# Kernel optimization log

Measured on AMD Instinct MI355X. Metric: run time of the kernel, lower is better.

Reference implementation:

```python
import jax, jax.numpy as jnp
import numpy as np

N_NODES = 100000
N_EDGES = 1600000
N_GRAPHS = 256
IN_C = 64
HID = 128
OUT = 128
BN_EPS = 1e-5


def setup_inputs() -> dict:
    key = jax.random.key(0)
    ks = jax.random.split(key, 24)
    x = jax.random.normal(ks[0], (N_NODES, IN_C), jnp.float32)
    edge_index = jax.random.randint(ks[1], (2, N_EDGES), 0, N_NODES, dtype=jnp.int64 if jax.config.jax_enable_x64 else jnp.int32)
    batch = jnp.sort(jax.random.randint(ks[2], (N_NODES,), 0, N_GRAPHS))

    def lin(k, i, o):
        return (jax.random.normal(k, (i, o), jnp.float32) / np.float32(np.sqrt(i)))

    d = {"x": x, "edge_index": edge_index, "batch": batch}
    in_dims = [IN_C, HID, HID]
    for l in range(3):
        d[f"w1_{l}"] = lin(ks[3 + 6 * l], in_dims[l], HID)
        d[f"b1_{l}"] = jnp.zeros((HID,), jnp.float32)
        d[f"w2_{l}"] = lin(ks[4 + 6 * l], HID, HID)
        d[f"b2_{l}"] = jnp.zeros((HID,), jnp.float32)
        d[f"gamma_{l}"] = jnp.ones((HID,), jnp.float32)
        d[f"beta_{l}"] = jnp.zeros((HID,), jnp.float32)
    d["proj_w"] = lin(ks[22], HID, OUT)
    d["proj_b"] = jnp.zeros((OUT,), jnp.float32)
    return d


def _gin_forward(x, edge_index, batch, layers, proj_w, proj_b):
    src, dst = edge_index[0], edge_index[1]
    h = x
    for (w1, b1, w2, b2, g, b) in layers:
        # GINConv (eps=0, aggr='add'): MLP(h_i + sum_{j->i} h_j)
        agg = jax.ops.segment_sum(h[src], dst, num_segments=h.shape[0])
        z = h + agg
        z = jax.nn.relu(z @ w1 + b1) @ w2 + b2
        # BatchNorm1d, training mode (biased batch stats)
        mean = z.mean(axis=0)
        var = z.var(axis=0)
        z = (z - mean) * jax.lax.rsqrt(var + BN_EPS) * g + b
        h = jax.nn.relu(z)
    # global_mean_pool over graph ids
    s = jax.ops.segment_sum(h, batch, num_segments=N_GRAPHS)
    cnt = jax.ops.segment_sum(jnp.ones((h.shape[0], 1), h.dtype), batch, num_segments=N_GRAPHS)
    hg = s / jnp.maximum(cnt, 1.0)
    return hg @ proj_w + proj_b


def reference(x, edge_index, batch,
              w1_0, b1_0, w2_0, b2_0, gamma_0, beta_0,
              w1_1, b1_1, w2_1, b2_1, gamma_1, beta_1,
              w1_2, b1_2, w2_2, b2_2, gamma_2, beta_2,
              proj_w, proj_b):
    layers = [
        (w1_0, b1_0, w2_0, b2_0, gamma_0, beta_0),
        (w1_1, b1_1, w2_1, b2_1, gamma_1, beta_1),
        (w1_2, b1_2, w2_2, b2_2, gamma_2, beta_2),
    ]
    return _gin_forward(x, edge_index, batch, layers, proj_w, proj_b)
```

## Files before the change

kernel.cpp:

```cpp
#include <hip/hip_runtime.h>

#define N_NODES 100000
#define N_EDGES 1600000
#define N_GRAPHS 256
#define HID 128
#define BN_EPS 1e-5f

#define NT 1563
#define EB 4096
#define RB 391
#define MB 1563

typedef __bf16 bf16x8 __attribute__((ext_vector_type(8)));
typedef __bf16 bf16x4 __attribute__((ext_vector_type(4)));
typedef __bf16 bf16x2 __attribute__((ext_vector_type(2)));
typedef float f32x4 __attribute__((ext_vector_type(4)));

__global__ __launch_bounds__(256) void setup_kernel(
    const float* __restrict__ x, __bf16* __restrict__ xb,
    const float* __restrict__ wa, const float* __restrict__ wb,
    const float* __restrict__ wc, const float* __restrict__ wd,
    const float* __restrict__ we, const float* __restrict__ wf,
    __bf16* __restrict__ wt,
    const int* __restrict__ batch, int* __restrict__ counts) {
  int b = blockIdx.x;
  if (b < 6250) {
    int idx = b * 256 + threadIdx.x;
    if (idx >= N_NODES * 16) return;
    f32x4 v = ((const f32x4*)x)[idx];
    bf16x4 o = {(__bf16)v[0], (__bf16)v[1], (__bf16)v[2], (__bf16)v[3]};
    ((bf16x4*)xb)[idx] = o;
  } else if (b < 6250 + 352) {
    int idx = (b - 6250) * 256 + threadIdx.x;
    if (idx >= 90112) return;
    const float* w;
    int K, local;
    if (idx < 8192) { w = wa; K = 64; local = idx; }
    else {
      int s = (idx - 8192) / 16384;
      local = (idx - 8192) - s * 16384;
      K = 128;
      w = (s == 0) ? wb : (s == 1) ? wc : (s == 2) ? wd : (s == 3) ? we : wf;
    }
    int n = local / K, k = local - n * K;
    wt[idx] = (__bf16)w[k * 128 + n];
  } else {
    int t = (b - 6602) * 256 + threadIdx.x;
    int r0 = t * 64;
    if (r0 >= N_NODES) return;
    int rend = min(r0 + 64, N_NODES);
    int curg = batch[r0], cnt = 0;
    for (int r = r0; r < rend; r++) {
      int g = batch[r];
      if (g != curg) {
        atomicAdd(&counts[curg], cnt);
        curg = g;
        cnt = 1;
      } else {
        cnt++;
      }
    }
    atomicAdd(&counts[curg], cnt);
  }
}

__global__ __launch_bounds__(256) void tile_hist_kernel(const int* __restrict__ ei,
                                                        int* __restrict__ tcnt) {
  __shared__ int hist[NT];
  int t = threadIdx.x;
  for (int i = t; i < NT; i += 256) hist[i] = 0;
  __syncthreads();
  int base = blockIdx.x * EB;
#pragma unroll 4
  for (int i = 0; i < EB / 256; i++) {
    int e = base + i * 256 + t;
    if (e < N_EDGES) atomicAdd(&hist[ei[N_EDGES + e] >> 6], 1);
  }
  __syncthreads();
  for (int i = t; i < NT; i += 256) {
    int h = hist[i];
    if (h) atomicAdd(&tcnt[i], h);
  }
}

__global__ __launch_bounds__(256) void tile_scan_kernel(const int* __restrict__ tcnt,
                                                        int* __restrict__ tstart,
                                                        int* __restrict__ gcursor) {
  __shared__ int ps[256];
  int t = threadIdx.x;
  const int CH = (NT + 255) / 256;
  int lo = t * CH, hi = min(lo + CH, NT);
  int s = 0;
  for (int i = lo; i < hi; i++) s += tcnt[i];
  ps[t] = s;
  __syncthreads();
  for (int off = 1; off < 256; off <<= 1) {
    int v = ps[t];
    int u = (t >= off) ? ps[t - off] : 0;
    __syncthreads();
    ps[t] = v + u;
    __syncthreads();
  }
  int base = (t == 0) ? 0 : ps[t - 1];
  for (int i = lo; i < hi; i++) {
    tstart[i] = base;
    gcursor[i] = base;
    base += tcnt[i];
  }
  if (t == 0) tstart[NT] = N_EDGES;
}

__global__ __launch_bounds__(256) void reorder2_kernel(const int* __restrict__ ei,
                                                       int* __restrict__ gcursor,
                                                       int* __restrict__ epack) {
  __shared__ int hist[NT];
  int t = threadIdx.x;
  for (int i = t; i < NT; i += 256) hist[i] = 0;
  __syncthreads();
  int base = blockIdx.x * EB;
#pragma unroll 4
  for (int i = 0; i < EB / 256; i++) {
    int e = base + i * 256 + t;
    if (e < N_EDGES) atomicAdd(&hist[ei[N_EDGES + e] >> 6], 1);
  }
  __syncthreads();
  for (int i = t; i < NT; i += 256) {
    int h = hist[i];
    if (h) hist[i] = atomicAdd(&gcursor[i], h);
  }
  __syncthreads();
#pragma unroll 4
  for (int i = 0; i < EB / 256; i++) {
    int e = base + i * 256 + t;
    if (e < N_EDGES) {
      int d = ei[N_EDGES + e];
      int s = ei[e];
      int pos = atomicAdd(&hist[d >> 6], 1);
      epack[pos] = (s << 6) | (d & 63);
    }
  }
}

__global__ __launch_bounds__(256) void row_sort_kernel(const int* __restrict__ tstart,
                                                       const int* __restrict__ epack,
                                                       int* __restrict__ starts,
                                                       int* __restrict__ srcs) {
  __shared__ int cnt[64];
  __shared__ int rbase[65];
  __shared__ int rofs[64];
  int t = threadIdx.x, b = blockIdx.x;
  int ts = tstart[b], te = tstart[b + 1];
  if (t < 64) cnt[t] = 0;
  __syncthreads();
  for (int i = ts + t; i < te; i += 256) atomicAdd(&cnt[epack[i] & 63], 1);
  __syncthreads();
  if (t == 0) {
    int a = 0;
    for (int r = 0; r < 64; r++) { rbase[r] = a; a += cnt[r]; }
    rbase[64] = a;
  }
  __syncthreads();
  if (t < 64) rofs[t] = ts + rbase[t];
  if (t <= 64) {
    int gr = b * 64 + t;
    if (gr <= N_NODES) starts[gr] = ts + rbase[t];
  }
  __syncthreads();
  for (int i = ts + t; i < te; i += 256) {
    int p = epack[i];
    int pos = atomicAdd(&rofs[p & 63], 1);
    srcs[pos] = p >> 6;
  }
}

template <int C, bool BN>
__global__ __launch_bounds__(256) void gather_kernel(const __bf16* __restrict__ h,
                                                     const float* __restrict__ bnab,
                                                     const int* __restrict__ starts,
                                                     const int* __restrict__ srcs,
                                                     __bf16* __restrict__ z) {
  const int lane = threadIdx.x & 63;
  const int row = __builtin_amdgcn_readfirstlane(blockIdx.x * 4 + (threadIdx.x >> 6));
  const int e0 = starts[row], e1 = starts[row + 1];

  if constexpr (C == 128) {
    float a0 = 0.f, a1 = 0.f, b0 = 0.f, b1 = 0.f;
    if constexpr (BN) {
      a0 = bnab[lane * 2];
      a1 = bnab[lane * 2 + 1];
      b0 = bnab[HID + lane * 2];
      b1 = bnab[HID + lane * 2 + 1];
    }
#define ACCBN(vv, ss)                                                  \
    do {                                                               \
      if constexpr (BN) {                                              \
        ss.x += fmaxf(fmaf(a0, (float)(vv)[0], b0), 0.f);              \
        ss.y += fmaxf(fmaf(a1, (float)(vv)[1], b1), 0.f);              \
      } else {                                                         \
        ss.x += (float)(vv)[0];                                        \
        ss.y += (float)(vv)[1];                                        \
      }                                                                \
    } while (0)
    float2 s0 = {0.f, 0.f}, s1 = {0.f, 0.f}, s2 = {0.f, 0.f}, s3 = {0.f, 0.f};
    int e = e0;
    for (; e + 3 < e1; e += 4) {
      int i0 = srcs[e];
      int i1 = srcs[e + 1];
      int i2 = srcs[e + 2];
      int i3 = srcs[e + 3];
      bf16x2 v0 = *(const bf16x2*)(h + (size_t)i0 * 128 + lane * 2);
      bf16x2 v1 = *(const bf16x2*)(h + (size_t)i1 * 128 + lane * 2);
      bf16x2 v2 = *(const bf16x2*)(h + (size_t)i2 * 128 + lane * 2);
      bf16x2 v3 = *(const bf16x2*)(h + (size_t)i3 * 128 + lane * 2);
      ACCBN(v0, s0);
      ACCBN(v1, s1);
      ACCBN(v2, s2);
      ACCBN(v3, s3);
    }
    for (; e < e1; e++) {
      int i0 = srcs[e];
      bf16x2 vv = *(const bf16x2*)(h + (size_t)i0 * 128 + lane * 2);
      ACCBN(vv, s0);
    }
    bf16x2 sv = *(const bf16x2*)(h + (size_t)row * 128 + lane * 2);
    ACCBN(sv, s0);
    float tx = (s0.x + s1.x) + (s2.x + s3.x);
    float ty = (s0.y + s1.y) + (s2.y + s3.y);
    bf16x2 o = {(__bf16)tx, (__bf16)ty};
    *(bf16x2*)(z + (size_t)row * 128 + lane * 2) = o;
#undef ACCBN
  } else {
    float s0 = 0.f, s1 = 0.f, s2 = 0.f, s3 = 0.f;
    int e = e0;
    for (; e + 3 < e1; e += 4) {
      int i0 = srcs[e];
      int i1 = srcs[e + 1];
      int i2 = srcs[e + 2];
      int i3 = srcs[e + 3];
      float v0 = (float)h[(size_t)i0 * 64 + lane];
      float v1 = (float)h[(size_t)i1 * 64 + lane];
      float v2 = (float)h[(size_t)i2 * 64 + lane];
      float v3 = (float)h[(size_t)i3 * 64 + lane];
      s0 += v0; s1 += v1; s2 += v2; s3 += v3;
    }
    for (; e < e1; e++) {
      int i0 = srcs[e];
      s0 += (float)h[(size_t)i0 * 64 + lane];
    }
    s0 += (float)h[(size_t)row * 64 + lane];
    float tot = (s0 + s1) + (s2 + s3);
    z[(size_t)row * 64 + lane] = (__bf16)tot;
  }
}

template <int CIN>
__global__ __launch_bounds__(256) void mlp_kernel(
    const __bf16* __restrict__ z, const __bf16* __restrict__ w1t,
    const float* __restrict__ b1, const __bf16* __restrict__ w2t,
    const float* __restrict__ b2, __bf16* __restrict__ u,
    float* __restrict__ part) {
  constexpr int TS = HID + 8;
  __shared__ __align__(16) __bf16 sm[64 * TS];

  const int t = threadIdx.x;
  const int wave = t >> 6;
  const int lane = t & 63;
  const int l16 = lane & 15;
  const int quad = lane >> 4;
  const int rowbase = blockIdx.x * 64;
  const int nvalid = min(64, N_NODES - rowbase);
  const int arow = min(rowbase + wave * 16 + l16, N_NODES - 1);

  const f32x4 zero4 = {0.f, 0.f, 0.f, 0.f};
  f32x4 acc[8];

  {
    bf16x8 af[CIN / 32];
    const __bf16* ap = z + (size_t)arow * CIN + quad * 8;
#pragma unroll
    for (int ks = 0; ks < CIN / 32; ks++) af[ks] = *(const bf16x8*)(ap + ks * 32);
#pragma unroll
    for (int ct = 0; ct < 8; ct++) acc[ct] = zero4;
#pragma unroll
    for (int ks = 0; ks < CIN / 32; ks++) {
#pragma unroll
      for (int ct = 0; ct < 8; ct++) {
        bf16x8 bfr = *(const bf16x8*)(w1t + (ct * 16 + l16) * CIN + ks * 32 + quad * 8);
        acc[ct] = __builtin_amdgcn_mfma_f32_16x16x32_bf16(af[ks], bfr, acc[ct], 0, 0, 0);
      }
    }
#pragma unroll
    for (int ct = 0; ct < 8; ct++) {
      int col = ct * 16 + l16;
      float bias = b1[col];
#pragma unroll
      for (int r = 0; r < 4; r++) {
        float v = acc[ct][r] + bias;
        sm[(wave * 16 + quad * 4 + r) * TS + col] = (__bf16)(v > 0.f ? v : 0.f);
      }
    }
  }

  {
#pragma unroll
    for (int ct = 0; ct < 8; ct++) acc[ct] = zero4;
    const __bf16* arowp = sm + (wave * 16 + l16) * TS + quad * 8;
#pragma unroll
    for (int ks = 0; ks < HID / 32; ks++) {
      bf16x8 af = *(const bf16x8*)(arowp + ks * 32);
#pragma unroll
      for (int ct = 0; ct < 8; ct++) {
        bf16x8 bfr = *(const bf16x8*)(w2t + (ct * 16 + l16) * HID + ks * 32 + quad * 8);
        acc[ct] = __builtin_amdgcn_mfma_f32_16x16x32_bf16(af, bfr, acc[ct], 0, 0, 0);
      }
    }
#pragma unroll
    for (int ct = 0; ct < 8; ct++) {
      int col = ct * 16 + l16;
      float bias = b2[col];
#pragma unroll
      for (int r = 0; r < 4; r++) {
        sm[(wave * 16 + quad * 4 + r) * TS + col] = (__bf16)(acc[ct][r] + bias);
      }
    }
  }
  __syncthreads();

  for (int f = t; f < 64 * 16; f += 256) {
    int r = f >> 4, c8 = f & 15;
    if (r < nvalid) {
      bf16x8 v = *(const bf16x8*)(sm + r * TS + c8 * 8);
      *(bf16x8*)(u + (size_t)(rowbase + r) * HID + c8 * 8) = v;
    }
  }
  if (t < HID) {
    float s = 0.f, sq = 0.f;
    for (int r = 0; r < nvalid; r++) {
      float v = (float)sm[r * TS + t];
      s += v;
      sq += v * v;
    }
    part[(size_t)blockIdx.x * 256 + t] = s;
    part[(size_t)blockIdx.x * 256 + HID + t] = sq;
  }
}

__global__ __launch_bounds__(256) void bn_stats_kernel(const float* __restrict__ part,
                                                       const float* __restrict__ gamma,
                                                       const float* __restrict__ beta,
                                                       float* __restrict__ bnab) {
  __shared__ float ss[256], qq[256];
  int c = blockIdx.x;
  int t = threadIdx.x;
  float s = 0.f, q = 0.f;
  for (int b = t; b < MB; b += 256) {
    s += part[(size_t)b * 256 + c];
    q += part[(size_t)b * 256 + HID + c];
  }
  ss[t] = s; qq[t] = q;
  __syncthreads();
  for (int off = 128; off > 0; off >>= 1) {
    if (t < off) { ss[t] += ss[t + off]; qq[t] += qq[t + off]; }
    __syncthreads();
  }
  if (t == 0) {
    const float invN = 1.f / (float)N_NODES;
    float mean = ss[0] * invN;
    float var = qq[0] * invN - mean * mean;
    float a = gamma[c] * rsqrtf(var + BN_EPS);
    bnab[c] = a;
    bnab[HID + c] = beta[c] - mean * a;
  }
}

__global__ __launch_bounds__(128) void bn_apply_pool_kernel(const __bf16* __restrict__ u,
                                                            const float* __restrict__ bnab,
                                                            const int* __restrict__ batch,
                                                            float* __restrict__ pool) {
  int c = threadIdx.x;
  int r0 = blockIdx.x * 64;
  if (r0 >= N_NODES) return;
  int rend = min(r0 + 64, N_NODES);
  float a = bnab[c], b = bnab[HID + c];
  float accv = 0.f;
  int curg = -1;
  for (int r = r0; r < rend; r++) {
    int g = batch[r];
    if (g != curg) {
      if (curg >= 0) atomicAdd(&pool[curg * HID + c], accv);
      curg = g;
      accv = 0.f;
    }
    float v = (float)u[(size_t)r * HID + c];
    v = v * a + b;
    accv += (v > 0.f ? v : 0.f);
  }
  if (curg >= 0) atomicAdd(&pool[curg * HID + c], accv);
}

__global__ __launch_bounds__(128) void pool_proj_kernel(const float* __restrict__ pool,
                                                        const int* __restrict__ counts,
                                                        const float* __restrict__ pw,
                                                        const float* __restrict__ pb,
                                                        float* __restrict__ out) {
  int g = blockIdx.x;
  int c = threadIdx.x;
  __shared__ float hg[HID];
  float cnt = (float)max(counts[g], 1);
  hg[c] = pool[g * HID + c] / cnt;
  __syncthreads();
  float acc = pb[c];
#pragma unroll 8
  for (int k = 0; k < HID; k++) acc += hg[k] * pw[k * HID + c];
  out[g * HID + c] = acc;
}

extern "C" void kernel_launch(void* const* d_in, const int* in_sizes, int n_in,
                              void* d_out, int out_size, void* d_ws, size_t ws_size,
                              hipStream_t stream) {
  (void)in_sizes; (void)n_in; (void)out_size; (void)ws_size;
  const float* x = (const float*)d_in[0];
  const int* ei = (const int*)d_in[1];
  const int* batch = (const int*)d_in[2];
  const float* w1[3] = {(const float*)d_in[3], (const float*)d_in[9], (const float*)d_in[15]};
  const float* b1[3] = {(const float*)d_in[4], (const float*)d_in[10], (const float*)d_in[16]};
  const float* w2[3] = {(const float*)d_in[5], (const float*)d_in[11], (const float*)d_in[17]};
  const float* b2[3] = {(const float*)d_in[6], (const float*)d_in[12], (const float*)d_in[18]};
  const float* gm[3] = {(const float*)d_in[7], (const float*)d_in[13], (const float*)d_in[19]};
  const float* bt[3] = {(const float*)d_in[8], (const float*)d_in[14], (const float*)d_in[20]};
  const float* pw = (const float*)d_in[21];
  const float* pb = (const float*)d_in[22];
  float* out = (float*)d_out;

  char* ws = (char*)d_ws;
  __bf16* bufA = (__bf16*)ws;        ws += (size_t)N_NODES * HID * 2;
  __bf16* bufB = (__bf16*)ws;        ws += (size_t)N_NODES * HID * 2;
  __bf16* bufC = (__bf16*)ws;        ws += (size_t)N_NODES * HID * 2;
  __bf16* z0 = (__bf16*)ws;          ws += (size_t)N_NODES * 64 * 2;
  __bf16* xb = (__bf16*)ws;          ws += (size_t)N_NODES * 64 * 2;
  int* srcs = (int*)ws;              ws += (size_t)N_EDGES * 4;
  int* epack = (int*)ws;             ws += (size_t)N_EDGES * 4;
  int* starts = (int*)ws;            ws += (size_t)(N_NODES + 1) * 4;
  int* tcnt = (int*)ws;              ws += NT * 4;
  int* tstart = (int*)ws;            ws += (NT + 1) * 4;
  int* gcursor = (int*)ws;           ws += NT * 4;
  ws = (char*)(((uintptr_t)ws + 63) & ~(uintptr_t)63);
  float* part = (float*)ws;          ws += (size_t)MB * 256 * 4;
  __bf16* wt_all = (__bf16*)ws;      ws += 90112 * 2;
  ws = (char*)(((uintptr_t)ws + 63) & ~(uintptr_t)63);
  float* bnab = (float*)ws;          ws += 256 * 4;
  float* pool = (float*)ws;          ws += N_GRAPHS * HID * 4;
  int* counts = (int*)ws;            ws += N_GRAPHS * 4;

  __bf16* w1t0 = wt_all;
  __bf16* w2t0 = wt_all + 8192;
  __bf16* w1t1 = wt_all + 24576;
  __bf16* w2t1 = wt_all + 40960;
  __bf16* w1t2 = wt_all + 57344;
  __bf16* w2t2 = wt_all + 73728;

  const int gat_blocks = (N_NODES + 3) / 4;

  hipMemsetAsync(pool, 0, (size_t)N_GRAPHS * HID * 4 + N_GRAPHS * 4, stream);
  hipMemsetAsync(tcnt, 0, NT * 4, stream);

  setup_kernel<<<6609, 256, 0, stream>>>(x, xb, w1[0], w2[0], w1[1], w2[1],
                                         w1[2], w2[2], wt_all, batch, counts);

  tile_hist_kernel<<<RB, 256, 0, stream>>>(ei, tcnt);
  tile_scan_kernel<<<1, 256, 0, stream>>>(tcnt, tstart, gcursor);
  reorder2_kernel<<<RB, 256, 0, stream>>>(ei, gcursor, epack);
  row_sort_kernel<<<NT, 256, 0, stream>>>(tstart, epack, starts, srcs);

  gather_kernel<64, false><<<gat_blocks, 256, 0, stream>>>(xb, nullptr, starts, srcs, z0);
  mlp_kernel<64><<<MB, 256, 0, stream>>>(z0, w1t0, b1[0], w2t0, b2[0], bufA, part);
  bn_stats_kernel<<<HID, 256, 0, stream>>>(part, gm[0], bt[0], bnab);

  gather_kernel<128, true><<<gat_blocks, 256, 0, stream>>>(bufA, bnab, starts, srcs, bufC);
  mlp_kernel<128><<<MB, 256, 0, stream>>>(bufC, w1t1, b1[1], w2t1, b2[1], bufB, part);
  bn_stats_kernel<<<HID, 256, 0, stream>>>(part, gm[1], bt[1], bnab);

  gather_kernel<128, true><<<gat_blocks, 256, 0, stream>>>(bufB, bnab, starts, srcs, bufC);
  mlp_kernel<128><<<MB, 256, 0, stream>>>(bufC, w1t2, b1[2], w2t2, b2[2], bufA, part);
  bn_stats_kernel<<<HID, 256, 0, stream>>>(part, gm[2], bt[2], bnab);

  bn_apply_pool_kernel<<<MB, 128, 0, stream>>>(bufA, bnab, batch, pool);

  pool_proj_kernel<<<N_GRAPHS, 128, 0, stream>>>(pool, counts, pw, pb, out);
}
```

Baseline: 593.2 us.

## Shrink MLP blocks to one wave, compute BN stats in registers, atomic-reduce partials

The MLP kernel now runs one 64-thread wave per 16-row tile instead of four waves per 64 rows. It writes its output straight from the MFMA accumulators and reduces per-column sums with shuffles, which drops the shared-memory round trip and the block barrier. The per-channel BN stats kernel is replaced by a grid-stride partial reducer that atomically adds into a per-layer accumulator. Consumers (the gather and the pool kernel) now derive the scale and shift inline from those sums. The trade-offs are four times more partial rows to reduce, float atomics that make the sum order nondeterministic, and strided uncoalesced bf16 stores from the MFMA layout.

```diff
diff --git a/kernel.cpp b/kernel.cpp
--- a/kernel.cpp
+++ b/kernel.cpp
@@ -9,7 +9,7 @@
 #define NT 1563
 #define EB 4096
 #define RB 391
-#define MB 1563
+#define PB 6250
 
 typedef __bf16 bf16x8 __attribute__((ext_vector_type(8)));
 typedef __bf16 bf16x4 __attribute__((ext_vector_type(4)));
@@ -175,7 +175,9 @@
 
 template <int C, bool BN>
 __global__ __launch_bounds__(256) void gather_kernel(const __bf16* __restrict__ h,
-                                                     const float* __restrict__ bnab,
+                                                     const float* __restrict__ accum,
+                                                     const float* __restrict__ gamma,
+                                                     const float* __restrict__ beta,
                                                      const int* __restrict__ starts,
                                                      const int* __restrict__ srcs,
                                                      __bf16* __restrict__ z) {
@@ -186,10 +188,15 @@
   if constexpr (C == 128) {
     float a0 = 0.f, a1 = 0.f, b0 = 0.f, b1 = 0.f;
     if constexpr (BN) {
-      a0 = bnab[lane * 2];
-      a1 = bnab[lane * 2 + 1];
-      b0 = bnab[HID + lane * 2];
-      b1 = bnab[HID + lane * 2 + 1];
+      const int c0 = lane * 2, c1 = c0 + 1;
+      const float invN = 1.f / (float)N_NODES;
+      float m0 = accum[c0] * invN, m1 = accum[c1] * invN;
+      float v0 = accum[HID + c0] * invN - m0 * m0;
+      float v1 = accum[HID + c1] * invN - m1 * m1;
+      a0 = gamma[c0] * rsqrtf(v0 + BN_EPS);
+      a1 = gamma[c1] * rsqrtf(v1 + BN_EPS);
+      b0 = beta[c0] - m0 * a0;
+      b1 = beta[c1] - m1 * a1;
     }
 #define ACCBN(vv, ss)                                                  \
     do {                                                               \
@@ -254,29 +261,25 @@
 }
 
 template <int CIN>
-__global__ __launch_bounds__(256) void mlp_kernel(
+__global__ __launch_bounds__(64) void mlp_kernel(
     const __bf16* __restrict__ z, const __bf16* __restrict__ w1t,
     const float* __restrict__ b1, const __bf16* __restrict__ w2t,
     const float* __restrict__ b2, __bf16* __restrict__ u,
     float* __restrict__ part) {
   constexpr int TS = HID + 8;
-  __shared__ __align__(16) __bf16 sm[64 * TS];
-
-  const int t = threadIdx.x;
-  const int wave = t >> 6;
-  const int lane = t & 63;
+  __shared__ __align__(16) __bf16 sm[16 * TS];
+
+  const int lane = threadIdx.x;
   const int l16 = lane & 15;
   const int quad = lane >> 4;
-  const int rowbase = blockIdx.x * 64;
-  const int nvalid = min(64, N_NODES - rowbase);
-  const int arow = min(rowbase + wave * 16 + l16, N_NODES - 1);
+  const int rowbase = blockIdx.x * 16;
 
   const f32x4 zero4 = {0.f, 0.f, 0.f, 0.f};
   f32x4 acc[8];
 
   {
     bf16x8 af[CIN / 32];
-    const __bf16* ap = z + (size_t)arow * CIN + quad * 8;
+    const __bf16* ap = z + (size_t)(rowbase + l16) * CIN + quad * 8;
 #pragma unroll
     for (int ks = 0; ks < CIN / 32; ks++) af[ks] = *(const bf16x8*)(ap + ks * 32);
 #pragma unroll
@@ -296,7 +299,7 @@
 #pragma unroll
       for (int r = 0; r < 4; r++) {
         float v = acc[ct][r] + bias;
-        sm[(wave * 16 + quad * 4 + r) * TS + col] = (__bf16)(v > 0.f ? v : 0.f);
+        sm[(quad * 4 + r) * TS + col] = (__bf16)(v > 0.f ? v : 0.f);
       }
     }
   }
@@ -304,7 +307,7 @@
   {
 #pragma unroll
     for (int ct = 0; ct < 8; ct++) acc[ct] = zero4;
-    const __bf16* arowp = sm + (wave * 16 + l16) * TS + quad * 8;
+    const __bf16* arowp = sm + l16 * TS + quad * 8;
 #pragma unroll
     for (int ks = 0; ks < HID / 32; ks++) {
       bf16x8 af = *(const bf16x8*)(arowp + ks * 32);
@@ -314,74 +317,57 @@
         acc[ct] = __builtin_amdgcn_mfma_f32_16x16x32_bf16(af, bfr, acc[ct], 0, 0, 0);
       }
     }
-#pragma unroll
-    for (int ct = 0; ct < 8; ct++) {
-      int col = ct * 16 + l16;
-      float bias = b2[col];
-#pragma unroll
-      for (int r = 0; r < 4; r++) {
-        sm[(wave * 16 + quad * 4 + r) * TS + col] = (__bf16)(acc[ct][r] + bias);
-      }
-    }
-  }
-  __syncthreads();
-
-  for (int f = t; f < 64 * 16; f += 256) {
-    int r = f >> 4, c8 = f & 15;
-    if (r < nvalid) {
-      bf16x8 v = *(const bf16x8*)(sm + r * TS + c8 * 8);
-      *(bf16x8*)(u + (size_t)(rowbase + r) * HID + c8 * 8) = v;
-    }
-  }
-  if (t < HID) {
-    float s = 0.f, sq = 0.f;
-    for (int r = 0; r < nvalid; r++) {
-      float v = (float)sm[r * TS + t];
-      s += v;
-      sq += v * v;
-    }
-    part[(size_t)blockIdx.x * 256 + t] = s;
-    part[(size_t)blockIdx.x * 256 + HID + t] = sq;
-  }
-}
-
-__global__ __launch_bounds__(256) void bn_stats_kernel(const float* __restrict__ part,
-                                                       const float* __restrict__ gamma,
-                                                       const float* __restrict__ beta,
-                                                       float* __restrict__ bnab) {
-  __shared__ float ss[256], qq[256];
-  int c = blockIdx.x;
+  }
+
+#pragma unroll
+  for (int ct = 0; ct < 8; ct++) {
+    int col = ct * 16 + l16;
+    float bias = b2[col];
+    float s = 0.f, q = 0.f;
+#pragma unroll
+    for (int r = 0; r < 4; r++) {
+      float v = acc[ct][r] + bias;
+      __bf16 bv = (__bf16)v;
+      u[(size_t)(rowbase + quad * 4 + r) * HID + col] = bv;
+      float fv = (float)bv;
+      s += fv;
+      q += fv * fv;
+    }
+    s += __shfl_xor(s, 16);
+    s += __shfl_xor(s, 32);
+    q += __shfl_xor(q, 16);
+    q += __shfl_xor(q, 32);
+    if (quad == 0) {
+      part[(size_t)blockIdx.x * 256 + col] = s;
+      part[(size_t)blockIdx.x * 256 + HID + col] = q;
+    }
+  }
+}
+
+__global__ __launch_bounds__(256) void reduce_part_kernel(const float* __restrict__ part,
+                                                          float* __restrict__ accum) {
   int t = threadIdx.x;
-  float s = 0.f, q = 0.f;
-  for (int b = t; b < MB; b += 256) {
-    s += part[(size_t)b * 256 + c];
-    q += part[(size_t)b * 256 + HID + c];
-  }
-  ss[t] = s; qq[t] = q;
-  __syncthreads();
-  for (int off = 128; off > 0; off >>= 1) {
-    if (t < off) { ss[t] += ss[t + off]; qq[t] += qq[t + off]; }
-    __syncthreads();
-  }
-  if (t == 0) {
-    const float invN = 1.f / (float)N_NODES;
-    float mean = ss[0] * invN;
-    float var = qq[0] * invN - mean * mean;
-    float a = gamma[c] * rsqrtf(var + BN_EPS);
-    bnab[c] = a;
-    bnab[HID + c] = beta[c] - mean * a;
-  }
+  float s = 0.f;
+  for (int r = blockIdx.x; r < PB; r += gridDim.x)
+    s += part[(size_t)r * 256 + t];
+  atomicAdd(&accum[t], s);
 }
 
 __global__ __launch_bounds__(128) void bn_apply_pool_kernel(const __bf16* __restrict__ u,
-                                                            const float* __restrict__ bnab,
+                                                            const float* __restrict__ accum,
+                                                            const float* __restrict__ gamma,
+                                                            const float* __restrict__ beta,
                                                             const int* __restrict__ batch,
                                                             float* __restrict__ pool) {
   int c = threadIdx.x;
   int r0 = blockIdx.x * 64;
   if (r0 >= N_NODES) return;
   int rend = min(r0 + 64, N_NODES);
-  float a = bnab[c], b = bnab[HID + c];
+  const float invN = 1.f / (float)N_NODES;
+  float mean = accum[c] * invN;
+  float var = accum[HID + c] * invN - mean * mean;
+  float a = gamma[c] * rsqrtf(var + BN_EPS);
+  float b = beta[c] - mean * a;
   float accv = 0.f;
   int curg = -1;
   for (int r = r0; r < rend; r++) {
@@ -445,10 +431,10 @@
   int* tstart = (int*)ws;            ws += (NT + 1) * 4;
   int* gcursor = (int*)ws;           ws += NT * 4;
   ws = (char*)(((uintptr_t)ws + 63) & ~(uintptr_t)63);
-  float* part = (float*)ws;          ws += (size_t)MB * 256 * 4;
+  float* part = (float*)ws;          ws += (size_t)PB * 256 * 4;
   __bf16* wt_all = (__bf16*)ws;      ws += 90112 * 2;
   ws = (char*)(((uintptr_t)ws + 63) & ~(uintptr_t)63);
-  float* bnab = (float*)ws;          ws += 256 * 4;
+  float* accum = (float*)ws;         ws += 3 * 256 * 4;
   float* pool = (float*)ws;          ws += N_GRAPHS * HID * 4;
   int* counts = (int*)ws;            ws += N_GRAPHS * 4;
 
@@ -459,9 +445,13 @@
   __bf16* w1t2 = wt_all + 57344;
   __bf16* w2t2 = wt_all + 73728;
 
+  float* acc0 = accum;
+  float* acc1 = accum + 256;
+  float* acc2 = accum + 512;
+
   const int gat_blocks = (N_NODES + 3) / 4;
 
-  hipMemsetAsync(pool, 0, (size_t)N_GRAPHS * HID * 4 + N_GRAPHS * 4, stream);
+  hipMemsetAsync(accum, 0, 3 * 256 * 4 + (size_t)N_GRAPHS * HID * 4 + N_GRAPHS * 4, stream);
   hipMemsetAsync(tcnt, 0, NT * 4, stream);
 
   setup_kernel<<<6609, 256, 0, stream>>>(x, xb, w1[0], w2[0], w1[1], w2[1],
@@ -472,19 +462,22 @@
   reorder2_kernel<<<RB, 256, 0, stream>>>(ei, gcursor, epack);
   row_sort_kernel<<<NT, 256, 0, stream>>>(tstart, epack, starts, srcs);
 
-  gather_kernel<64, false><<<gat_blocks, 256, 0, stream>>>(xb, nullptr, starts, srcs, z0);
-  mlp_kernel<64><<<MB, 256, 0, stream>>>(z0, w1t0, b1[0], w2t0, b2[0], bufA, part);
-  bn_stats_kernel<<<HID, 256, 0, stream>>>(part, gm[0], bt[0], bnab);
-
-  gather_kernel<128, true><<<gat_blocks, 256, 0, stream>>>(bufA, bnab, starts, srcs, bufC);
-  mlp_kernel<128><<<MB, 256, 0, stream>>>(bufC, w1t1, b1[1], w2t1, b2[1], bufB, part);
-  bn_stats_kernel<<<HID, 256, 0, stream>>>(part, gm[1], bt[1], bnab);
-
-  gather_kernel<128, true><<<gat_blocks, 256, 0, stream>>>(bufB, bnab, starts, srcs, bufC);
-  mlp_kernel<128><<<MB, 256, 0, stream>>>(bufC, w1t2, b1[2], w2t2, b2[2], bufA, part);
-  bn_stats_kernel<<<HID, 256, 0, stream>>>(part, gm[2], bt[2], bnab);
-
-  bn_apply_pool_kernel<<<MB, 128, 0, stream>>>(bufA, bnab, batch, pool);
+  gather_kernel<64, false><<<gat_blocks, 256, 0, stream>>>(xb, nullptr, nullptr, nullptr,
+                                                           starts, srcs, z0);
+  mlp_kernel<64><<<PB, 64, 0, stream>>>(z0, w1t0, b1[0], w2t0, b2[0], bufA, part);
+  reduce_part_kernel<<<128, 256, 0, stream>>>(part, acc0);
+
+  gather_kernel<128, true><<<gat_blocks, 256, 0, stream>>>(bufA, acc0, gm[0], bt[0],
+                                                           starts, srcs, bufC);
+  mlp_kernel<128><<<PB, 64, 0, stream>>>(bufC, w1t1, b1[1], w2t1, b2[1], bufB, part);
+  reduce_part_kernel<<<128, 256, 0, stream>>>(part, acc1);
+
+  gather_kernel<128, true><<<gat_blocks, 256, 0, stream>>>(bufB, acc1, gm[1], bt[1],
+                                                           starts, srcs, bufC);
+  mlp_kernel<128><<<PB, 64, 0, stream>>>(bufC, w1t2, b1[2], w2t2, b2[2], bufA, part);
+  reduce_part_kernel<<<128, 256, 0, stream>>>(part, acc2);
+
+  bn_apply_pool_kernel<<<NT, 128, 0, stream>>>(bufA, acc2, gm[2], bt[2], batch, pool);
 
   pool_proj_kernel<<<N_GRAPHS, 128, 0, stream>>>(pool, counts, pw, pb, out);
 }
```

New measurement: 612.8 us. +3.3%, slower.
